# Kernel optimization log

Hardware: AMD Instinct MI355X
Metric: run time of the kernel (lower is better)

The kernel has to match this reference:

```python
import jax, jax.numpy as jnp
import numpy as np

D_K, D_MODEL, NUM_HEADS = 64, 1024, 16


def _xavier(key, shape):
    # xavier_uniform over last two dims (fan_in=shape[-2], fan_out=shape[-1])
    fan_in, fan_out = shape[-2], shape[-1]
    limit = float(np.sqrt(6.0 / (fan_in + fan_out)))
    return jax.random.uniform(key, shape, jnp.float32, -limit, limit)


def setup_inputs() -> dict:
    key = jax.random.key(0)
    kx, kq, kk, kv, ko = jax.random.split(key, 5)
    x = jax.random.normal(kx, (2, 2048, D_MODEL), dtype=jnp.float32)
    w_q = _xavier(kq, (NUM_HEADS, D_MODEL, D_K))
    w_k = _xavier(kk, (NUM_HEADS, D_MODEL, D_K))
    w_v = _xavier(kv, (NUM_HEADS, D_MODEL, D_K))
    w_o = _xavier(ko, (NUM_HEADS * D_K, D_MODEL))
    return {"x": x, "w_q": w_q, "w_k": w_k, "w_v": w_v, "w_o": w_o}


def reference(x, w_q, w_k, w_v, w_o):
    scale = 1.0 / jnp.sqrt(jnp.asarray(D_K, dtype=jnp.float32))
    q = jnp.einsum('bsd,hdk->bhsk', x, w_q)
    k = jnp.einsum('bsd,hdk->bhsk', x, w_k)
    v = jnp.einsum('bsd,hdk->bhsk', x, w_v)
    scores = jnp.einsum('bhqk,bhmk->bhqm', q, k) * scale  # [B,H,S,S]
    weights = jax.nn.softmax(scores, axis=-1)
    z = jnp.einsum('bhqm,bhmk->bhqk', weights, v)
    b, h, s, dk = z.shape
    z = jnp.transpose(z, (0, 2, 1, 3)).reshape(b, s, h * dk)
    z = jnp.einsum('bse,ed->bsd', z, w_o)
    return x + z  # dropout_prob=0.0 (eval): identity
```

## Files before the change

kernel.cpp:

```cpp
#include <hip/hip_runtime.h>
#include <hip/hip_bf16.h>
#include <stdint.h>

typedef float    f32x4  __attribute__((ext_vector_type(4)));
typedef __bf16   bf16x8 __attribute__((ext_vector_type(8)));
typedef __bf16   bf16x2 __attribute__((ext_vector_type(2)));
typedef uint16_t u16;

#define NHEADS 16
#define DKV    64
#define DMODEL 1024
#define BATCH  2
#define SEQ    2048
#define ROWS   4096

#define EXP2F(x) __builtin_amdgcn_exp2f(x)

__device__ __forceinline__ u16 f2bf(float f) {
  __bf16 h = (__bf16)f;
  union { __bf16 h; u16 u; } c; c.h = h; return c.u;
}
__device__ __forceinline__ uint32_t pk2(float a, float b) {
  union { bf16x2 v; uint32_t u; } c;
  c.v = (bf16x2){(__bf16)a, (__bf16)b};
  return c.u;
}

__device__ __forceinline__ void gload16(const void* g, void* l) {
  __builtin_amdgcn_global_load_lds(
      (const __attribute__((address_space(1))) uint32_t*)g,
      (__attribute__((address_space(3))) uint32_t*)l, 16, 0, 0);
}

__device__ __forceinline__ f32x4 mfma16(bf16x8 a, bf16x8 b, f32x4 c) {
  return __builtin_amdgcn_mfma_f32_16x16x32_bf16(a, b, c, 0, 0, 0);
}

__global__ void prep_kernel(const float* __restrict__ x, u16* __restrict__ xb,
                            const float* __restrict__ wq, const float* __restrict__ wk,
                            const float* __restrict__ wv, const float* __restrict__ wo,
                            u16* __restrict__ wt, u16* __restrict__ wot) {
  int blk = blockIdx.x, tid = threadIdx.x;
  if (blk < 2048) {
    int i = blk * 256 + tid;
    const float4* p = (const float4*)(x + (size_t)i * 8);
    float4 a = p[0], b = p[1];
    uint32_t o0 = pk2(a.x, a.y), o1 = pk2(a.z, a.w);
    uint32_t o2 = pk2(b.x, b.y), o3 = pk2(b.z, b.w);
    uint4 pk = make_uint4(o0, o1, o2, o3);
    *(uint4*)(xb + (size_t)i * 8) = pk;
    return;
  }
  __shared__ float t[64][65];
  int wblk = blk - 2048;
  const float* src; u16* dst; int sld, dld;
  if (wblk < 768) {
    int p = wblk >> 8, rem = wblk & 255;
    int h = rem >> 4, dt = rem & 15;
    const float* w = (p == 0) ? wq : (p == 1) ? wk : wv;
    src = w + ((size_t)h * 1024 + dt * 64) * 64;   sld = 64;
    dst = wt + ((size_t)(p * 1024 + h * 64)) * 1024 + dt * 64; dld = 1024;
  } else {
    int t2 = wblk - 768, rt = t2 >> 4, ct = t2 & 15;
    src = wo + (size_t)(rt * 64) * 1024 + ct * 64;  sld = 1024;
    dst = wot + (size_t)(ct * 64) * 1024 + rt * 64; dld = 1024;
  }
#pragma unroll
  for (int i = 0; i < 16; i++) {
    int e = tid + i * 256, r = e >> 6, c = e & 63;
    t[r][c] = src[(size_t)r * sld + c];
  }
  __syncthreads();
#pragma unroll
  for (int i = 0; i < 16; i++) {
    int e = tid + i * 256, r = e >> 6, c = e & 63;
    dst[(size_t)r * dld + c] = f2bf(t[c][r]);
  }
}

__global__ __launch_bounds__(256) void qkv_gemm(
    const u16* __restrict__ xb, const u16* __restrict__ wt,
    u16* __restrict__ qout, u16* __restrict__ kout, u16* __restrict__ vout) {
  __shared__ __align__(16) u16 As[128 * 32];
  __shared__ __align__(16) u16 Bs[128 * 32];
  int tid = threadIdx.x, l = tid & 63, w = tid >> 6;
  int cpx = gridDim.x >> 3;
  int bid = (blockIdx.x & 7) * cpx + (blockIdx.x >> 3);
  bool vpath = bid >= 512;
  const u16 *A, *Bt; int m0, n0;
  if (!vpath) { A = xb; Bt = wt; m0 = (bid >> 4) * 128; n0 = (bid & 15) * 128; }
  else { int b2 = bid - 512; A = wt + (size_t)2048 * 1024; Bt = xb;
         m0 = (b2 >> 5) * 128; n0 = (b2 & 31) * 128; }
  int wm = (w >> 1) * 64, wn = (w & 1) * 64;
  int cg = l >> 4, cl = l & 15;
  int lrow = l >> 2, lcol = l & 3;

  f32x4 acc[4][4];
#pragma unroll
  for (int i = 0; i < 4; i++)
#pragma unroll
    for (int j = 0; j < 4; j++) acc[i][j] = (f32x4){0.f, 0.f, 0.f, 0.f};

  for (int k0 = 0; k0 < 1024; k0 += 32) {
    __syncthreads();
    const u16* ga = A  + (size_t)(m0 + w * 16 + lrow) * 1024 + k0 + lcol * 8;
    const u16* gb = Bt + (size_t)(n0 + w * 16 + lrow) * 1024 + k0 + lcol * 8;
    gload16(ga,               &As[(w * 16) * 32]);
    gload16(ga + 64 * 1024,   &As[(w * 16 + 64) * 32]);
    gload16(gb,               &Bs[(w * 16) * 32]);
    gload16(gb + 64 * 1024,   &Bs[(w * 16 + 64) * 32]);
    __syncthreads();

    bf16x8 af[4], bfr[4];
#pragma unroll
    for (int mi = 0; mi < 4; mi++)
      af[mi] = *(const bf16x8*)&As[(wm + mi * 16 + cl) * 32 + cg * 8];
#pragma unroll
    for (int ni = 0; ni < 4; ni++)
      bfr[ni] = *(const bf16x8*)&Bs[(wn + ni * 16 + cl) * 32 + cg * 8];
#pragma unroll
    for (int mi = 0; mi < 4; mi++)
#pragma unroll
      for (int ni = 0; ni < 4; ni++)
        acc[mi][ni] = mfma16(af[mi], bfr[ni], acc[mi][ni]);
  }

#pragma unroll
  for (int mi = 0; mi < 4; mi++)
#pragma unroll
    for (int ni = 0; ni < 4; ni++) {
      int nbase = n0 + wn + ni * 16 + cl;
#pragma unroll
      for (int r = 0; r < 4; r++) {
        int m = m0 + wm + mi * 16 + cg * 4 + r;
        float v = acc[mi][ni][r];
        if (!vpath) {
          int p = nbase >> 10, hh = (nbase >> 6) & 15, dk = nbase & 63;
          int b = m >> 11, s = m & 2047;
          size_t o = ((size_t)(b * 16 + hh) * 2048 + s) * 64 + dk;
          if (p == 0) qout[o] = f2bf(v * 0.18033688f);
          else        kout[o] = f2bf(v);
        } else {
          vout[(size_t)m * 4096 + nbase] = f2bf(v);
        }
      }
    }
}

__global__ __launch_bounds__(256) void out_gemm(
    const u16* __restrict__ A, const u16* __restrict__ Bt,
    const float* __restrict__ xres, float* __restrict__ fout) {
  __shared__ __align__(16) u16 As[128 * 32];
  __shared__ __align__(16) u16 Bs[64 * 32];
  int tid = threadIdx.x, l = tid & 63, w = tid >> 6;
  int cpx = gridDim.x >> 3;
  int bid = (blockIdx.x & 7) * cpx + (blockIdx.x >> 3);
  int m0 = (bid >> 4) * 128, n0 = (bid & 15) * 64;
  int wm = (w >> 1) * 64, wn = (w & 1) * 32;
  int cg = l >> 4, cl = l & 15;
  int lrow = l >> 2, lcol = l & 3;

  f32x4 acc[4][2];
#pragma unroll
  for (int i = 0; i < 4; i++)
#pragma unroll
    for (int j = 0; j < 2; j++) acc[i][j] = (f32x4){0.f, 0.f, 0.f, 0.f};

  for (int k0 = 0; k0 < 1024; k0 += 32) {
    __syncthreads();
    const u16* ga = A  + (size_t)(m0 + w * 16 + lrow) * 1024 + k0 + lcol * 8;
    const u16* gb = Bt + (size_t)(n0 + w * 16 + lrow) * 1024 + k0 + lcol * 8;
    gload16(ga,             &As[(w * 16) * 32]);
    gload16(ga + 64 * 1024, &As[(w * 16 + 64) * 32]);
    gload16(gb,             &Bs[(w * 16) * 32]);
    __syncthreads();

    bf16x8 af[4], bfr[2];
#pragma unroll
    for (int mi = 0; mi < 4; mi++)
      af[mi] = *(const bf16x8*)&As[(wm + mi * 16 + cl) * 32 + cg * 8];
#pragma unroll
    for (int ni = 0; ni < 2; ni++)
      bfr[ni] = *(const bf16x8*)&Bs[(wn + ni * 16 + cl) * 32 + cg * 8];
#pragma unroll
    for (int mi = 0; mi < 4; mi++)
#pragma unroll
      for (int ni = 0; ni < 2; ni++)
        acc[mi][ni] = mfma16(af[mi], bfr[ni], acc[mi][ni]);
  }

#pragma unroll
  for (int mi = 0; mi < 4; mi++)
#pragma unroll
    for (int ni = 0; ni < 2; ni++) {
      int nbase = n0 + wn + ni * 16 + cl;
#pragma unroll
      for (int r = 0; r < 4; r++) {
        int m = m0 + wm + mi * 16 + cg * 4 + r;
        size_t o = (size_t)m * 1024 + nbase;
        fout[o] = acc[mi][ni][r] + xres[o];
      }
    }
}

__global__ __launch_bounds__(256) void attn_kernel(
    const u16* __restrict__ q, const u16* __restrict__ k,
    const u16* __restrict__ vt, u16* __restrict__ z) {
  __shared__ __align__(16) u16 Ks[2][64 * 64];
  __shared__ __align__(16) u16 Vs[2][64 * 64];
  __shared__ __align__(16) u16 Ps[4][32 * 64];
  int tid = threadIdx.x, l = tid & 63, w = tid >> 6;
  int blk = blockIdx.x;
  int xcd = blk & 7, slot = blk >> 3;
  int bh = xcd * 4 + (slot >> 4), qt = slot & 15;
  int b = bh >> 4, h = bh & 15;
  int q0 = qt * 128 + w * 32;
  int cg = l >> 4, cl = l & 15;
  int swz = (cl & 7) << 4;

  const u16* qb = q  + ((size_t)bh * 2048 + q0) * 64;
  const u16* kb = k  + (size_t)bh * 2048 * 64;
  const u16* vb = vt + (size_t)(h * 64) * 4096 + b * 2048;

  int srow = w * 16 + (l >> 3);
  int scb  = (l & 7) ^ (l >> 3);

  bf16x8 bq0[2], bq1[2];
#pragma unroll
  for (int qf = 0; qf < 2; qf++) {
    bq0[qf] = *(const bf16x8*)&qb[(size_t)(qf * 16 + cl) * 64 + cg * 8];
    bq1[qf] = *(const bf16x8*)&qb[(size_t)(qf * 16 + cl) * 64 + 32 + cg * 8];
  }

  f32x4 oacc[2][4];
#pragma unroll
  for (int qf = 0; qf < 2; qf++)
#pragma unroll
    for (int i = 0; i < 4; i++) oacc[qf][i] = (f32x4){0.f, 0.f, 0.f, 0.f};
  float lsum[2] = {0.f, 0.f};

  gload16(kb + (size_t)srow * 64 + scb * 8,         &Ks[0][(w * 16) * 64]);
  gload16(kb + (size_t)(srow + 8) * 64 + scb * 8,   &Ks[0][(w * 16 + 8) * 64]);
  gload16(vb + (size_t)srow * 4096 + scb * 8,       &Vs[0][(w * 16) * 64]);
  gload16(vb + (size_t)(srow + 8) * 4096 + scb * 8, &Vs[0][(w * 16 + 8) * 64]);
  __syncthreads();

  for (int t = 0; t < 32; t++) {
    int cur = t & 1, nxt = cur ^ 1;
    if (t + 1 < 32) {
      gload16(kb + ((size_t)(t + 1) * 64 + srow) * 64 + scb * 8,       &Ks[nxt][(w * 16) * 64]);
      gload16(kb + ((size_t)(t + 1) * 64 + srow + 8) * 64 + scb * 8,   &Ks[nxt][(w * 16 + 8) * 64]);
      gload16(vb + (size_t)srow * 4096 + (t + 1) * 64 + scb * 8,       &Vs[nxt][(w * 16) * 64]);
      gload16(vb + (size_t)(srow + 8) * 4096 + (t + 1) * 64 + scb * 8, &Vs[nxt][(w * 16 + 8) * 64]);
    }

    f32x4 sc[2][4];
    __builtin_amdgcn_s_setprio(1);
#pragma unroll
    for (int g = 0; g < 4; g++) {
      const char* kp = (const char*)&Ks[cur][(g * 16 + cl) * 64];
      bf16x8 a0 = *(const bf16x8*)(kp + ((cg * 16)      ^ swz));
      bf16x8 a1 = *(const bf16x8*)(kp + ((cg * 16 + 64) ^ swz));
#pragma unroll
      for (int qf = 0; qf < 2; qf++) {
        f32x4 t2 = (f32x4){-16.f, -16.f, -16.f, -16.f};
        t2 = mfma16(a0, bq0[qf], t2);
        t2 = mfma16(a1, bq1[qf], t2);
        sc[qf][g] = t2;
      }
    }
    __builtin_amdgcn_s_setprio(0);

#pragma unroll
    for (int qf = 0; qf < 2; qf++) {
      float rs = 0.f;
#pragma unroll
      for (int g = 0; g < 4; g++)
#pragma unroll
        for (int r = 0; r < 4; r++) {
          float p = EXP2F(sc[qf][g][r]);
          sc[qf][g][r] = p;
          rs += p;
        }
      lsum[qf] += rs;
    }

    bf16x8 pb0[2], pb1[2];
#pragma unroll
    for (int qf = 0; qf < 2; qf++) {
      char* pw = (char*)&Ps[w][(qf * 16 + cl) * 64];
#pragma unroll
      for (int g = 0; g < 4; g++) {
        uint32_t lo = pk2(sc[qf][g][0], sc[qf][g][1]);
        uint32_t hi = pk2(sc[qf][g][2], sc[qf][g][3]);
        *(uint2*)(pw + ((g * 32 + cg * 8) ^ swz)) = make_uint2(lo, hi);
      }
      pb0[qf] = *(const bf16x8*)(pw + ((cg * 16)      ^ swz));
      pb1[qf] = *(const bf16x8*)(pw + ((cg * 16 + 64) ^ swz));
    }

    __builtin_amdgcn_s_setprio(1);
#pragma unroll
    for (int nd = 0; nd < 4; nd++) {
      const char* vp = (const char*)&Vs[cur][(nd * 16 + cl) * 64];
      bf16x8 v0 = *(const bf16x8*)(vp + ((cg * 16)      ^ swz));
      bf16x8 v1 = *(const bf16x8*)(vp + ((cg * 16 + 64) ^ swz));
#pragma unroll
      for (int qf = 0; qf < 2; qf++) {
        oacc[qf][nd] = mfma16(v0, pb0[qf], oacc[qf][nd]);
        oacc[qf][nd] = mfma16(v1, pb1[qf], oacc[qf][nd]);
      }
    }
    __builtin_amdgcn_s_setprio(0);

    __syncthreads();
  }

#pragma unroll
  for (int qf = 0; qf < 2; qf++) {
    float ls = lsum[qf];
    ls += __shfl_xor(ls, 16);
    ls += __shfl_xor(ls, 32);
    float inv = 1.0f / ls;
    u16* zb = z + ((size_t)(b * 2048) + q0 + qf * 16 + cl) * 1024 + h * 64;
#pragma unroll
    for (int nd = 0; nd < 4; nd++) {
      uint32_t lo = pk2(oacc[qf][nd][0] * inv, oacc[qf][nd][1] * inv);
      uint32_t hi = pk2(oacc[qf][nd][2] * inv, oacc[qf][nd][3] * inv);
      *(uint2*)&zb[nd * 16 + cg * 4] = make_uint2(lo, hi);
    }
  }
}

extern "C" void kernel_launch(void* const* d_in, const int* in_sizes, int n_in,
                              void* d_out, int out_size, void* d_ws, size_t ws_size,
                              hipStream_t stream) {
  const float* x  = (const float*)d_in[0];
  const float* wq = (const float*)d_in[1];
  const float* wk = (const float*)d_in[2];
  const float* wv = (const float*)d_in[3];
  const float* wo = (const float*)d_in[4];
  float* out = (float*)d_out;

  uint8_t* ws = (uint8_t*)d_ws;
  u16* xb  = (u16*)(ws);
  u16* wt  = (u16*)(ws + (8ull  << 20));
  u16* wot = (u16*)(ws + (14ull << 20));
  u16* qb  = (u16*)(ws + (16ull << 20));
  u16* kb  = (u16*)(ws + (24ull << 20));
  u16* vt  = (u16*)(ws + (32ull << 20));
  u16* zb  = (u16*)(ws + (40ull << 20));
  if (ws_size < (48ull << 20)) return;

  prep_kernel<<<3072, 256, 0, stream>>>(x, xb, wq, wk, wv, wo, wt, wot);
  qkv_gemm<<<768, 256, 0, stream>>>(xb, wt, qb, kb, vt);
  attn_kernel<<<512, 256, 0, stream>>>(qb, kb, vt, zb);
  out_gemm<<<512, 256, 0, stream>>>(zb, wot, x, out);
}
```

Measured before the change: 193.1 us.

## Deepen GEMM K tiles with swizzled LDS and triple-buffer attention K/V

Both projection GEMMs now stage 64-wide K slices instead of 32 per iteration, using an XOR-swizzled LDS layout like the attention kernel's. This halves the number of barrier-separated K steps and is meant to avoid LDS bank conflicts on the wider rows. The attention kernel moves to a 4-slot K/V ring with a prefetch distance of two tiles and a barrier only every other iteration, to hide more global latency and cut synchronisation. The cost is larger LDS footprints: about 80 KB per attention block, which can lower occupancy, and more live fragment registers in the GEMMs.

```diff
diff --git a/kernel.cpp b/kernel.cpp
--- a/kernel.cpp
+++ b/kernel.cpp
@@ -81,8 +81,8 @@
 __global__ __launch_bounds__(256) void qkv_gemm(
     const u16* __restrict__ xb, const u16* __restrict__ wt,
     u16* __restrict__ qout, u16* __restrict__ kout, u16* __restrict__ vout) {
-  __shared__ __align__(16) u16 As[128 * 32];
-  __shared__ __align__(16) u16 Bs[128 * 32];
+  __shared__ __align__(16) u16 As[128 * 64];
+  __shared__ __align__(16) u16 Bs[128 * 64];
   int tid = threadIdx.x, l = tid & 63, w = tid >> 6;
   int cpx = gridDim.x >> 3;
   int bid = (blockIdx.x & 7) * cpx + (blockIdx.x >> 3);
@@ -93,7 +93,8 @@
          m0 = (b2 >> 5) * 128; n0 = (b2 & 31) * 128; }
   int wm = (w >> 1) * 64, wn = (w & 1) * 64;
   int cg = l >> 4, cl = l & 15;
-  int lrow = l >> 2, lcol = l & 3;
+  int scb = (l & 7) ^ (l >> 3);
+  int swz = (cl & 7) << 4;
 
   f32x4 acc[4][4];
 #pragma unroll
@@ -101,28 +102,37 @@
 #pragma unroll
     for (int j = 0; j < 4; j++) acc[i][j] = (f32x4){0.f, 0.f, 0.f, 0.f};
 
-  for (int k0 = 0; k0 < 1024; k0 += 32) {
+  for (int k0 = 0; k0 < 1024; k0 += 64) {
     __syncthreads();
-    const u16* ga = A  + (size_t)(m0 + w * 16 + lrow) * 1024 + k0 + lcol * 8;
-    const u16* gb = Bt + (size_t)(n0 + w * 16 + lrow) * 1024 + k0 + lcol * 8;
-    gload16(ga,               &As[(w * 16) * 32]);
-    gload16(ga + 64 * 1024,   &As[(w * 16 + 64) * 32]);
-    gload16(gb,               &Bs[(w * 16) * 32]);
-    gload16(gb + 64 * 1024,   &Bs[(w * 16 + 64) * 32]);
+    const u16* ga = A  + (size_t)(m0 + w * 32 + (l >> 3)) * 1024 + k0 + scb * 8;
+    const u16* gb = Bt + (size_t)(n0 + w * 32 + (l >> 3)) * 1024 + k0 + scb * 8;
+#pragma unroll
+    for (int j = 0; j < 4; j++) {
+      gload16(ga + (size_t)(j * 8) * 1024, &As[(w * 32 + j * 8) * 64]);
+      gload16(gb + (size_t)(j * 8) * 1024, &Bs[(w * 32 + j * 8) * 64]);
+    }
     __syncthreads();
 
-    bf16x8 af[4], bfr[4];
+    bf16x8 af[4][2], bfr[4][2];
+#pragma unroll
+    for (int mi = 0; mi < 4; mi++) {
+      const char* ap = (const char*)&As[(wm + mi * 16 + cl) * 64];
+      af[mi][0] = *(const bf16x8*)(ap + ((cg * 16)      ^ swz));
+      af[mi][1] = *(const bf16x8*)(ap + ((64 + cg * 16) ^ swz));
+    }
+#pragma unroll
+    for (int ni = 0; ni < 4; ni++) {
+      const char* bp = (const char*)&Bs[(wn + ni * 16 + cl) * 64];
+      bfr[ni][0] = *(const bf16x8*)(bp + ((cg * 16)      ^ swz));
+      bfr[ni][1] = *(const bf16x8*)(bp + ((64 + cg * 16) ^ swz));
+    }
 #pragma unroll
     for (int mi = 0; mi < 4; mi++)
-      af[mi] = *(const bf16x8*)&As[(wm + mi * 16 + cl) * 32 + cg * 8];
-#pragma unroll
-    for (int ni = 0; ni < 4; ni++)
-      bfr[ni] = *(const bf16x8*)&Bs[(wn + ni * 16 + cl) * 32 + cg * 8];
-#pragma unroll
-    for (int mi = 0; mi < 4; mi++)
-#pragma unroll
-      for (int ni = 0; ni < 4; ni++)
-        acc[mi][ni] = mfma16(af[mi], bfr[ni], acc[mi][ni]);
+#pragma unroll
+      for (int ni = 0; ni < 4; ni++) {
+        acc[mi][ni] = mfma16(af[mi][0], bfr[ni][0], acc[mi][ni]);
+        acc[mi][ni] = mfma16(af[mi][1], bfr[ni][1], acc[mi][ni]);
+      }
   }
 
 #pragma unroll
@@ -150,15 +160,16 @@
 __global__ __launch_bounds__(256) void out_gemm(
     const u16* __restrict__ A, const u16* __restrict__ Bt,
     const float* __restrict__ xres, float* __restrict__ fout) {
-  __shared__ __align__(16) u16 As[128 * 32];
-  __shared__ __align__(16) u16 Bs[64 * 32];
+  __shared__ __align__(16) u16 As[128 * 64];
+  __shared__ __align__(16) u16 Bs[64 * 64];
   int tid = threadIdx.x, l = tid & 63, w = tid >> 6;
   int cpx = gridDim.x >> 3;
   int bid = (blockIdx.x & 7) * cpx + (blockIdx.x >> 3);
   int m0 = (bid >> 4) * 128, n0 = (bid & 15) * 64;
   int wm = (w >> 1) * 64, wn = (w & 1) * 32;
   int cg = l >> 4, cl = l & 15;
-  int lrow = l >> 2, lcol = l & 3;
+  int scb = (l & 7) ^ (l >> 3);
+  int swz = (cl & 7) << 4;
 
   f32x4 acc[4][2];
 #pragma unroll
@@ -166,27 +177,38 @@
 #pragma unroll
     for (int j = 0; j < 2; j++) acc[i][j] = (f32x4){0.f, 0.f, 0.f, 0.f};
 
-  for (int k0 = 0; k0 < 1024; k0 += 32) {
+  for (int k0 = 0; k0 < 1024; k0 += 64) {
     __syncthreads();
-    const u16* ga = A  + (size_t)(m0 + w * 16 + lrow) * 1024 + k0 + lcol * 8;
-    const u16* gb = Bt + (size_t)(n0 + w * 16 + lrow) * 1024 + k0 + lcol * 8;
-    gload16(ga,             &As[(w * 16) * 32]);
-    gload16(ga + 64 * 1024, &As[(w * 16 + 64) * 32]);
-    gload16(gb,             &Bs[(w * 16) * 32]);
+    const u16* ga = A  + (size_t)(m0 + w * 32 + (l >> 3)) * 1024 + k0 + scb * 8;
+    const u16* gb = Bt + (size_t)(n0 + w * 16 + (l >> 3)) * 1024 + k0 + scb * 8;
+#pragma unroll
+    for (int j = 0; j < 4; j++)
+      gload16(ga + (size_t)(j * 8) * 1024, &As[(w * 32 + j * 8) * 64]);
+#pragma unroll
+    for (int j = 0; j < 2; j++)
+      gload16(gb + (size_t)(j * 8) * 1024, &Bs[(w * 16 + j * 8) * 64]);
     __syncthreads();
 
-    bf16x8 af[4], bfr[2];
+    bf16x8 af[4][2], bfr[2][2];
+#pragma unroll
+    for (int mi = 0; mi < 4; mi++) {
+      const char* ap = (const char*)&As[(wm + mi * 16 + cl) * 64];
+      af[mi][0] = *(const bf16x8*)(ap + ((cg * 16)      ^ swz));
+      af[mi][1] = *(const bf16x8*)(ap + ((64 + cg * 16) ^ swz));
+    }
+#pragma unroll
+    for (int ni = 0; ni < 2; ni++) {
+      const char* bp = (const char*)&Bs[(wn + ni * 16 + cl) * 64];
+      bfr[ni][0] = *(const bf16x8*)(bp + ((cg * 16)      ^ swz));
+      bfr[ni][1] = *(const bf16x8*)(bp + ((64 + cg * 16) ^ swz));
+    }
 #pragma unroll
     for (int mi = 0; mi < 4; mi++)
-      af[mi] = *(const bf16x8*)&As[(wm + mi * 16 + cl) * 32 + cg * 8];
-#pragma unroll
-    for (int ni = 0; ni < 2; ni++)
-      bfr[ni] = *(const bf16x8*)&Bs[(wn + ni * 16 + cl) * 32 + cg * 8];
-#pragma unroll
-    for (int mi = 0; mi < 4; mi++)
-#pragma unroll
-      for (int ni = 0; ni < 2; ni++)
-        acc[mi][ni] = mfma16(af[mi], bfr[ni], acc[mi][ni]);
+#pragma unroll
+      for (int ni = 0; ni < 2; ni++) {
+        acc[mi][ni] = mfma16(af[mi][0], bfr[ni][0], acc[mi][ni]);
+        acc[mi][ni] = mfma16(af[mi][1], bfr[ni][1], acc[mi][ni]);
+      }
   }
 
 #pragma unroll
@@ -206,13 +228,13 @@
 __global__ __launch_bounds__(256) void attn_kernel(
     const u16* __restrict__ q, const u16* __restrict__ k,
     const u16* __restrict__ vt, u16* __restrict__ z) {
-  __shared__ __align__(16) u16 Ks[2][64 * 64];
-  __shared__ __align__(16) u16 Vs[2][64 * 64];
+  __shared__ __align__(16) u16 Ks[4][64 * 64];
+  __shared__ __align__(16) u16 Vs[4][64 * 64];
   __shared__ __align__(16) u16 Ps[4][32 * 64];
   int tid = threadIdx.x, l = tid & 63, w = tid >> 6;
   int blk = blockIdx.x;
-  int xcd = blk & 7, slot = blk >> 3;
-  int bh = xcd * 4 + (slot >> 4), qt = slot & 15;
+  int xcd = blk & 7, slot0 = blk >> 3;
+  int bh = xcd * 4 + (slot0 >> 4), qt = slot0 & 15;
   int b = bh >> 4, h = bh & 15;
   int q0 = qt * 128 + w * 32;
   int cg = l >> 4, cl = l & 15;
@@ -239,19 +261,23 @@
     for (int i = 0; i < 4; i++) oacc[qf][i] = (f32x4){0.f, 0.f, 0.f, 0.f};
   float lsum[2] = {0.f, 0.f};
 
-  gload16(kb + (size_t)srow * 64 + scb * 8,         &Ks[0][(w * 16) * 64]);
-  gload16(kb + (size_t)(srow + 8) * 64 + scb * 8,   &Ks[0][(w * 16 + 8) * 64]);
-  gload16(vb + (size_t)srow * 4096 + scb * 8,       &Vs[0][(w * 16) * 64]);
-  gload16(vb + (size_t)(srow + 8) * 4096 + scb * 8, &Vs[0][(w * 16 + 8) * 64]);
+#pragma unroll
+  for (int tt = 0; tt < 2; tt++) {
+    gload16(kb + ((size_t)tt * 64 + srow) * 64 + scb * 8,       &Ks[tt][(w * 16) * 64]);
+    gload16(kb + ((size_t)tt * 64 + srow + 8) * 64 + scb * 8,   &Ks[tt][(w * 16 + 8) * 64]);
+    gload16(vb + (size_t)srow * 4096 + tt * 64 + scb * 8,       &Vs[tt][(w * 16) * 64]);
+    gload16(vb + (size_t)(srow + 8) * 4096 + tt * 64 + scb * 8, &Vs[tt][(w * 16 + 8) * 64]);
+  }
   __syncthreads();
 
   for (int t = 0; t < 32; t++) {
-    int cur = t & 1, nxt = cur ^ 1;
-    if (t + 1 < 32) {
-      gload16(kb + ((size_t)(t + 1) * 64 + srow) * 64 + scb * 8,       &Ks[nxt][(w * 16) * 64]);
-      gload16(kb + ((size_t)(t + 1) * 64 + srow + 8) * 64 + scb * 8,   &Ks[nxt][(w * 16 + 8) * 64]);
-      gload16(vb + (size_t)srow * 4096 + (t + 1) * 64 + scb * 8,       &Vs[nxt][(w * 16) * 64]);
-      gload16(vb + (size_t)(srow + 8) * 4096 + (t + 1) * 64 + scb * 8, &Vs[nxt][(w * 16 + 8) * 64]);
+    int cur = t & 3;
+    if (t + 2 < 32) {
+      int ns = (t + 2) & 3;
+      gload16(kb + ((size_t)(t + 2) * 64 + srow) * 64 + scb * 8,       &Ks[ns][(w * 16) * 64]);
+      gload16(kb + ((size_t)(t + 2) * 64 + srow + 8) * 64 + scb * 8,   &Ks[ns][(w * 16 + 8) * 64]);
+      gload16(vb + (size_t)srow * 4096 + (t + 2) * 64 + scb * 8,       &Vs[ns][(w * 16) * 64]);
+      gload16(vb + (size_t)(srow + 8) * 4096 + (t + 2) * 64 + scb * 8, &Vs[ns][(w * 16 + 8) * 64]);
     }
 
     f32x4 sc[2][4];
@@ -313,7 +339,7 @@
     }
     __builtin_amdgcn_s_setprio(0);
 
-    __syncthreads();
+    if (t & 1) __syncthreads();
   }
 
 #pragma unroll
```

Measured after the change: 191.5 us. No clear change (-0.8%).
